# Kernel optimization log

Hardware: AMD Instinct MI355X
Metric: run time of the kernel (lower is better)

The kernel has to match this reference:

```python
import jax, jax.numpy as jnp
import numpy as np

L = 768          # temporal feature length
C_IN = 2048      # feature channels
NA = 10          # anchor scales per position
NC = 21          # num classes (20 + bg)
PRE_NMS = 1024   # pre-NMS top-k
POST_NMS = 128   # fixed proposal count after NMS
NMS_THR = 0.7
SCALE = 1.0      # cfg.Process.new_dilation*new_cluster/Frame
ANCHOR_SIZES = np.array([2., 4., 5., 6., 8., 9., 10., 12., 14., 16.], np.float32)


def _conv(x, w, b, pad=0):
    # x: [N,C,T], w: [O,I,K]
    y = jax.lax.conv_general_dilated(x, w, (1,), [(pad, pad)],
                                     dimension_numbers=('NCH', 'OIH', 'NCH'))
    return y + b[None, :, None]


def _lin(x, w, b):
    return x @ w.T + b


def _forward(feature, p):
    f = _conv(feature, p['w1f'], p['b1f'], 1)
    f = _conv(f, p['w2f'], p['b2f'], 1)
    x = _conv(f, p['wc1'], p['bc1'], 0)                      # [1,512,L]
    # SegmentProposal tower (relu only after conv4, as in source)
    h = _conv(x, p['sp1w'], p['sp1b'], 1)
    h = _conv(h, p['sp2w'], p['sp2b'], 1)
    h = _conv(h, p['sp3w'], p['sp3b'], 1)
    h = jax.nn.relu(_conv(h, p['sp4w'], p['sp4b'], 1))
    cls_score = _conv(h, p['spcw'], p['spcb'], 0)            # [1,2*NA,L]
    seg_pred = _conv(h, p['spsw'], p['spsb'], 0)             # [1,2*NA,L]

    def _resh(t):  # [1,2NA,L] -> [L*NA,2]  (transpose(2,1).view(B,L,C/2,2))
        return jnp.transpose(t, (0, 2, 1)).reshape(-1, 2)

    cls2 = _resh(cls_score)
    cls_prob = jax.nn.softmax(cls2, -1)
    off2 = _resh(seg_pred)

    # anchors: (center, half_len) per position per scale, position-major
    centers = (jnp.arange(L, dtype=jnp.float32) + 0.5) * SCALE
    halves = jnp.asarray(ANCHOR_SIZES) * 0.5
    a_c = jnp.repeat(centers, NA)
    a_h = jnp.tile(halves, L)
    im_info = L * SCALE

    # apply offsets: center shift + log-length scale, clip to video extent
    c = a_c + off2[:, 0] * (2.0 * a_h)
    hl = a_h * jnp.exp(off2[:, 1])
    s = jnp.clip(c - hl, 0.0, im_info)
    e = jnp.clip(c + hl, 0.0, im_info)
    scores = cls_prob[:, 1]

    top_sc, top_i = jax.lax.top_k(scores, PRE_NMS)
    ss, ee = s[top_i], e[top_i]

    def body(i, keep):
        inter = jnp.maximum(0., jnp.minimum(ee, ee[i]) - jnp.maximum(ss, ss[i]))
        union = (ee - ss) + (ee[i] - ss[i]) - inter
        iou = inter / jnp.maximum(union, 1e-8)
        sup = (iou > NMS_THR) & (jnp.arange(PRE_NMS) > i) & keep[i]
        return keep & ~sup

    keep = jax.lax.fori_loop(0, PRE_NMS, body, jnp.ones(PRE_NMS, bool))
    order = jnp.argsort((~keep).astype(jnp.int32), stable=True)  # kept first, score order
    sel = order[:POST_NMS]
    pidx = top_i[sel]
    ps, pe = s[pidx], e[pidx]
    pbbox = jnp.stack([(ps + pe) * 0.5, (pe - ps) * 0.5], -1)    # (center, half)

    # map proposals to feature index range (floor/ceil + clamp, as in source)
    st = jnp.clip(jnp.floor((pbbox[:, 0] - pbbox[:, 1]) / SCALE), 0, L - 1).astype(jnp.int32)
    en = jnp.clip(jnp.ceil((pbbox[:, 0] + pbbox[:, 1]) / SCALE), 0, L - 1).astype(jnp.int32)
    en = jnp.maximum(en, st)

    feat = f[0]                                              # [C_IN, L]
    tpos = jnp.arange(L)
    bins = jnp.arange(7)

    def roi_pool(se):  # AdaptiveMaxPool1d(7) over feat[:, s0:e0+1]
        s0, e0 = se
        ln = e0 - s0 + 1
        bs = s0 + (bins * ln) // 7
        be = s0 + ((bins + 1) * ln + 6) // 7 - 1
        m = (tpos[None, :] >= bs[:, None]) & (tpos[None, :] <= be[:, None])  # [7,L]
        v = jnp.where(m[None], feat[:, None, :], -jnp.inf)   # [C_IN,7,L]
        return v.max(-1)                                     # [C_IN,7]

    spp = jax.lax.map(roi_pool, (st, en))                    # [K,C_IN,7]

    y = _conv(spp, p['wc2'], p['bc2'], 0)
    y = _conv(y, p['w3'], p['b3'], 1)
    y = jax.nn.relu(_conv(y, p['w4'], p['b4'], 1))
    y = _conv(y, p['w5'], p['b5'], 1)
    y = jax.nn.relu(_conv(y, p['w6'], p['b6'], 1))
    y = y.reshape(y.shape[0], -1)                            # [K, 512*7]
    y = _lin(y, p['fc1w'], p['fc1b'])
    # Relation attention is computed but unused in the source forward -> omitted
    y = jax.nn.relu(y)
    y = _lin(y, p['fc2w'], p['fc2b'])
    y = _lin(y, p['fc3w'], p['fc3b'])
    obj_cls = _lin(y, p['clsw'], p['clsb'])                  # [K,NC]
    obj_off = _lin(y, p['boxw'], p['boxb']).reshape(-1, NC - 1, 2)
    cls_sel = cls2[pidx]                                     # [K,2]
    off_sel = off2[pidx]                                     # [K,2]
    return cls_sel, off_sel, obj_cls, obj_off


_PARAM_SHAPES = {
    'w1f': (2048, 2048, 3), 'b1f': (2048,),
    'w2f': (2048, 2048, 3), 'b2f': (2048,),
    'wc1': (512, 2048, 1), 'bc1': (512,),
    'sp1w': (512, 512, 3), 'sp1b': (512,),
    'sp2w': (512, 512, 3), 'sp2b': (512,),
    'sp3w': (512, 512, 3), 'sp3b': (512,),
    'sp4w': (512, 512, 3), 'sp4b': (512,),
    'spcw': (2 * NA, 512, 1), 'spcb': (2 * NA,),
    'spsw': (2 * NA, 512, 1), 'spsb': (2 * NA,),
    'wc2': (512, 2048, 1), 'bc2': (512,),
    'w3': (512, 512, 3), 'b3': (512,),
    'w4': (512, 512, 3), 'b4': (512,),
    'w5': (512, 512, 3), 'b5': (512,),
    'w6': (512, 512, 3), 'b6': (512,),
    'fc1w': (512, 512 * 7), 'fc1b': (512,),
    'fc2w': (256, 512), 'fc2b': (256,),
    'fc3w': (128, 256), 'fc3b': (128,),
    'clsw': (NC, 128), 'clsb': (NC,),
    'boxw': (2 * (NC - 1), 128), 'boxb': (2 * (NC - 1),),
}


def setup_inputs() -> dict:
    key = jax.random.key(0)
    inp = {'feature': jax.random.normal(jax.random.fold_in(key, 0), (1, C_IN, L), jnp.float32)}
    for i, (name, shp) in enumerate(sorted(_PARAM_SHAPES.items())):
        k = jax.random.fold_in(key, i + 1)
        inp[name] = jax.random.normal(k, shp, jnp.float32) * 0.02
    return inp


def reference(feature, b1f, b2f, b3, b4, b5, b6, bc1, bc2, boxb, boxw, clsb, clsw,
              fc1b, fc1w, fc2b, fc2w, fc3b, fc3w, sp1b, sp1w, sp2b, sp2w, sp3b, sp3w,
              sp4b, sp4w, spcb, spcw, spsb, spsw, w1f, w2f, w3, w4, w5, w6,
              wc1, wc2):
    p = dict(w1f=w1f, b1f=b1f, w2f=w2f, b2f=b2f, wc1=wc1, bc1=bc1,
             sp1w=sp1w, sp1b=sp1b, sp2w=sp2w, sp2b=sp2b, sp3w=sp3w, sp3b=sp3b,
             sp4w=sp4w, sp4b=sp4b, spcw=spcw, spcb=spcb, spsw=spsw, spsb=spsb,
             wc2=wc2, bc2=bc2, w3=w3, b3=b3, w4=w4, b4=b4, w5=w5, b5=b5,
             w6=w6, b6=b6, fc1w=fc1w, fc1b=fc1b, fc2w=fc2w, fc2b=fc2b,
             fc3w=fc3w, fc3b=fc3b, clsw=clsw, clsb=clsb, boxw=boxw, boxb=boxb)
    return _forward(feature, p)
```

## Files before the change

kernel.cpp:

```cpp
#include <hip/hip_runtime.h>

typedef __attribute__((ext_vector_type(8))) short short8;
typedef __attribute__((ext_vector_type(4))) float float4v;

__device__ __forceinline__ float bf(unsigned short u) {
    return __uint_as_float(((unsigned int)u) << 16);
}
__device__ __forceinline__ unsigned short f2b(float f) {
    unsigned int u = __float_as_uint(f);
    unsigned int r = (u + 0x7FFFu + ((u >> 16) & 1u)) >> 16;
    return (unsigned short)r;
}

__constant__ float c_anchors[10] = {2.f,4.f,5.f,6.f,8.f,9.f,10.f,12.f,14.f,16.f};

__global__ __launch_bounds__(256) void zeroXt_kernel(unsigned short* __restrict__ Xt, int CI) {
    int i = blockIdx.x * 256 + threadIdx.x;
    if (i < 2 * CI) {
        int row = (i >= CI) ? 769 : 0;
        int co = (i >= CI) ? (i - CI) : i;
        Xt[(size_t)row * CI + co] = 0;
        Xt[(size_t)770 * CI + (size_t)row * CI + co] = 0;
    }
}

__global__ __launch_bounds__(256) void decomp_kernel(const float* __restrict__ src,
                                                     unsigned short* __restrict__ Xt, int CI) {
    __shared__ float T[32][33];
    int l0 = blockIdx.x * 32, ci0 = blockIdx.y * 32;
    int tid = threadIdx.x;
#pragma unroll
    for (int i = 0; i < 4; i++) {
        int slot = tid + 256 * i;
        int r = slot >> 5, c = slot & 31;
        T[r][c] = src[(size_t)(ci0 + r) * 768 + l0 + c];
    }
    __syncthreads();
    unsigned short* Xh = Xt;
    unsigned short* Xl = Xt + (size_t)770 * CI;
#pragma unroll
    for (int i = 0; i < 4; i++) {
        int slot = tid + 256 * i;
        int li = slot >> 5, cc = slot & 31;
        float v = T[cc][li];
        unsigned short h = f2b(v);
        float lo = v - bf(h);
        size_t o = (size_t)(l0 + li + 1) * CI + ci0 + cc;
        Xh[o] = h;
        Xl[o] = f2b(lo);
    }
}

template <int TAPS, int SEGM>
__global__ __launch_bounds__(512, 6) void convmm_kernel(const float* __restrict__ W,
                                                        const unsigned short* __restrict__ Xt,
                                                        float* __restrict__ G,
                                                        int CO, int CI, int S, int NCOL, int planeElems) {
    constexpr int RS = TAPS * 32 + 8;
    constexpr int BROWS = SEGM ? 168 : 130;
    __shared__ unsigned short At[2][64 * RS];
    __shared__ unsigned short Bt[2][BROWS * 40];
    int tid = threadIdx.x;
    int lane = tid & 63, wid = tid >> 6;
    int q = lane >> 4, ln = lane & 15;
    int co0 = blockIdx.x * 64;
    int c0 = blockIdx.y * 128;
    int s = blockIdx.z;
    int kPer = CI / S, cis = s * kPer;
    const unsigned short* Xh = Xt;
    const unsigned short* Xl = Xt + planeElems;
    int row0 = SEGM ? ((c0 / 7) * 9 + c0 % 7) : c0;

    float4v zero4 = {0.f, 0.f, 0.f, 0.f};
    float4v acc[2][2];
    acc[0][0] = zero4; acc[0][1] = zero4; acc[1][0] = zero4; acc[1][1] = zero4;

    int wave_m = (wid >> 2) * 32;
    int wave_n = (wid & 3) * 32;

    int rowb[2];
#pragma unroll
    for (int nf = 0; nf < 2; nf++) {
        int col = c0 + wave_n + nf * 16 + ln;
        rowb[nf] = SEGM ? ((col / 7) * 9 + col % 7 - row0) : (wave_n + nf * 16 + ln);
    }

    for (int kb = 0; kb < kPer; kb += 32) {
        int cib = cis + kb;
        if (TAPS == 3) {
#pragma unroll
            for (int i = 0; i < 2; i++) {
                int slot = tid + 512 * i;
                int row = slot >> 4, cc0 = (slot & 15) * 2;
                const float* wp = W + ((size_t)(co0 + row) * CI + cib + cc0) * 3;
                float fa[6];
#pragma unroll
                for (int j = 0; j < 6; j++) fa[j] = wp[j];
#pragma unroll
                for (int t = 0; t < 3; t++) {
                    unsigned short h0 = f2b(fa[t]);
                    unsigned short h1 = f2b(fa[t + 3]);
                    unsigned short e0 = f2b(fa[t] - bf(h0));
                    unsigned short e1 = f2b(fa[t + 3] - bf(h1));
                    *(unsigned int*)&At[0][row * RS + t * 32 + cc0] =
                        (unsigned int)h0 | ((unsigned int)h1 << 16);
                    *(unsigned int*)&At[1][row * RS + t * 32 + cc0] =
                        (unsigned int)e0 | ((unsigned int)e1 << 16);
                }
            }
        } else {
            int row = tid >> 3, cc0 = (tid & 7) * 4;
            float4 wv = *(const float4*)(W + (size_t)(co0 + row) * CI + cib + cc0);
            float fa[4] = {wv.x, wv.y, wv.z, wv.w};
            unsigned short h[4], e[4];
#pragma unroll
            for (int j = 0; j < 4; j++) {
                h[j] = f2b(fa[j]);
                e[j] = f2b(fa[j] - bf(h[j]));
            }
            unsigned long long hp = (unsigned long long)h[0] | ((unsigned long long)h[1] << 16) |
                                    ((unsigned long long)h[2] << 32) | ((unsigned long long)h[3] << 48);
            unsigned long long ep = (unsigned long long)e[0] | ((unsigned long long)e[1] << 16) |
                                    ((unsigned long long)e[2] << 32) | ((unsigned long long)e[3] << 48);
            *(unsigned long long*)&At[0][row * RS + cc0] = hp;
            *(unsigned long long*)&At[1][row * RS + cc0] = ep;
        }
#pragma unroll
        for (int i = 0; i < 3; i++) {
            int slot = tid + 512 * i;
            if (slot < BROWS * 8) {
                int p = slot >= BROWS * 4 ? 1 : 0;
                int rem = slot - p * BROWS * 4;
                int r = rem >> 2, qq = rem & 3;
                const unsigned short* src = (p ? Xl : Xh) + (size_t)(row0 + r) * CI + cib + qq * 8;
                short8 v = *(const short8*)src;
                *(short8*)&Bt[p][r * 40 + qq * 8] = v;
            }
        }
        __syncthreads();
#pragma unroll
        for (int t = 0; t < TAPS; t++) {
            int shift = (TAPS == 1) ? 1 : t;
            short8 bh[2], bl[2];
#pragma unroll
            for (int nf = 0; nf < 2; nf++) {
                int rrow = rowb[nf] + shift;
                bh[nf] = *(const short8*)&Bt[0][rrow * 40 + q * 8];
                bl[nf] = *(const short8*)&Bt[1][rrow * 40 + q * 8];
            }
#pragma unroll
            for (int mf = 0; mf < 2; mf++) {
                int mrow = wave_m + mf * 16 + ln;
                short8 ah = *(const short8*)&At[0][mrow * RS + t * 32 + q * 8];
                short8 al = *(const short8*)&At[1][mrow * RS + t * 32 + q * 8];
#pragma unroll
                for (int nf = 0; nf < 2; nf++) {
                    acc[mf][nf] = __builtin_amdgcn_mfma_f32_16x16x32_bf16(ah, bh[nf], acc[mf][nf], 0, 0, 0);
                    acc[mf][nf] = __builtin_amdgcn_mfma_f32_16x16x32_bf16(ah, bl[nf], acc[mf][nf], 0, 0, 0);
                    acc[mf][nf] = __builtin_amdgcn_mfma_f32_16x16x32_bf16(al, bh[nf], acc[mf][nf], 0, 0, 0);
                }
            }
        }
        __syncthreads();
    }
    float* Gz = G + (size_t)s * CO * NCOL;
#pragma unroll
    for (int mf = 0; mf < 2; mf++)
#pragma unroll
        for (int nf = 0; nf < 2; nf++) {
            int col = c0 + wave_n + nf * 16 + ln;
            int rowb2 = co0 + wave_m + mf * 16 + q * 4;
#pragma unroll
            for (int r = 0; r < 4; r++)
                Gz[(size_t)(rowb2 + r) * NCOL + col] = acc[mf][nf][r];
        }
}

__global__ __launch_bounds__(256) void finsum_x_kernel(const float* __restrict__ G,
                                                       const float* __restrict__ bias,
                                                       unsigned short* __restrict__ Xt,
                                                       int CO, int P) {
    __shared__ float T[64][65];
    int co0 = blockIdx.x * 64, l0 = blockIdx.y * 64;
    int tid = threadIdx.x;
#pragma unroll 1
    for (int i = 0; i < 16; i++) {
        int slot = tid + 256 * i;
        int r = slot >> 6, c = slot & 63;
        float v = bias[co0 + r];
        for (int p = 0; p < P; p++) v += G[((size_t)p * CO + co0 + r) * 768 + l0 + c];
        T[r][c] = v;
    }
    __syncthreads();
    unsigned short* Xh = Xt;
    unsigned short* Xl = Xt + (size_t)770 * CO;
#pragma unroll 1
    for (int i = 0; i < 16; i++) {
        int slot = tid + 256 * i;
        int li = slot >> 6, ci = slot & 63;
        float v = T[ci][li];
        unsigned short h = f2b(v);
        float lo = v - bf(h);
        size_t o = (size_t)(l0 + li + 1) * CO + co0 + ci;
        Xh[o] = h;
        Xl[o] = f2b(lo);
    }
}

__global__ __launch_bounds__(256) void finsum_xf_kernel(const float* __restrict__ G,
                                                        const float* __restrict__ bias,
                                                        unsigned short* __restrict__ Xt,
                                                        float* __restrict__ outF,
                                                        int CO, int P) {
    __shared__ float T[64][65];
    int co0 = blockIdx.x * 64, l0 = blockIdx.y * 64;
    int tid = threadIdx.x;
#pragma unroll 1
    for (int i = 0; i < 16; i++) {
        int slot = tid + 256 * i;
        int r = slot >> 6, c = slot & 63;
        float v = bias[co0 + r];
        for (int p = 0; p < P; p++) v += G[((size_t)p * CO + co0 + r) * 768 + l0 + c];
        T[r][c] = v;
        outF[(size_t)(co0 + r) * 768 + l0 + c] = v;
    }
    __syncthreads();
    unsigned short* Xh = Xt;
    unsigned short* Xl = Xt + (size_t)770 * CO;
#pragma unroll 1
    for (int i = 0; i < 16; i++) {
        int slot = tid + 256 * i;
        int li = slot >> 6, ci = slot & 63;
        float v = T[ci][li];
        unsigned short h = f2b(v);
        float lo = v - bf(h);
        size_t o = (size_t)(l0 + li + 1) * CO + co0 + ci;
        Xh[o] = h;
        Xl[o] = f2b(lo);
    }
}

__global__ __launch_bounds__(256) void finsum_seg_kernel(const float* __restrict__ G,
                                                         const float* __restrict__ bias,
                                                         unsigned short* __restrict__ Xs,
                                                         int P, int relu) {
    __shared__ float T[64][65];
    int co0 = blockIdx.x * 64, c0 = blockIdx.y * 64;
    int tid = threadIdx.x;
#pragma unroll 1
    for (int i = 0; i < 16; i++) {
        int slot = tid + 256 * i;
        int r = slot >> 6, c = slot & 63;
        float v = bias[co0 + r];
        for (int p = 0; p < P; p++) v += G[((size_t)p * 512 + co0 + r) * 896 + c0 + c];
        if (relu) v = fmaxf(v, 0.f);
        T[r][c] = v;
    }
    __syncthreads();
    unsigned short* Xh = Xs;
    unsigned short* Xl = Xs + (size_t)1160 * 512;
#pragma unroll 1
    for (int i = 0; i < 16; i++) {
        int slot = tid + 256 * i;
        int li = slot >> 6, ci = slot & 63;
        float v = T[ci][li];
        int c = c0 + li;
        int row = (c / 7) * 9 + c % 7 + 1;
        unsigned short h = f2b(v);
        float lo = v - bf(h);
        size_t o = (size_t)row * 512 + co0 + ci;
        Xh[o] = h;
        Xl[o] = f2b(lo);
    }
}

__global__ __launch_bounds__(256) void finsum_f_kernel(const float* __restrict__ G,
                                                       const float* __restrict__ bias,
                                                       float* __restrict__ out,
                                                       int CO, int P, int ncol, int relu) {
    int i = blockIdx.x * 256 + threadIdx.x;
    if (i >= CO * ncol) return;
    int r = i / ncol, c = i - r * ncol;
    float v = bias[r];
    for (int p = 0; p < P; p++) v += G[((size_t)p * CO + r) * ncol + c];
    if (relu) v = fmaxf(v, 0.f);
    out[i] = v;
}

__global__ __launch_bounds__(256) void finalize_kernel(const float* __restrict__ part,
                                                       float* __restrict__ out,
                                                       const float* __restrict__ bias,
                                                       int RPAD, int R, int NCOLS, int S, int relu) {
    int i = blockIdx.x * 256 + threadIdx.x;
    int total = R * NCOLS;
    if (i >= total) return;
    int r = i / NCOLS;
    int c = i - r * NCOLS;
    float v = 0.f;
    for (int s = 0; s < S; s++) v += part[((size_t)s * RPAD + r) * NCOLS + c];
    v += bias[r];
    if (relu) v = fmaxf(v, 0.f);
    out[i] = v;
}

template <int MODE, int EPI>
__global__ __launch_bounds__(256) void gemm_kernel(const float* __restrict__ W,
                                                   const float* __restrict__ B,
                                                   const float* __restrict__ bias,
                                                   float* __restrict__ outF,
                                                   int R, int K, int NCOLS, int LDB, int S, int relu) {
    __shared__ __align__(16) float Bt[16][68];
    __shared__ __align__(16) float Wt[16][68];
    int tid = threadIdx.x;
    int tx = tid & 15, ty = tid >> 4;
    int r0 = blockIdx.x * 64, c0 = blockIdx.y * 64, s = blockIdx.z;
    int kPer = K / S;
    int k0s = s * kPer;
    float acc[4][4] = {};
    for (int kb = 0; kb < kPer; kb += 16) {
        int k0 = k0s + kb;
        {
            int rr = r0 + (tid >> 2);
            int q = tid & 3;
            float4 wv4 = {0.f, 0.f, 0.f, 0.f};
            if (rr < R) wv4 = *(const float4*)(W + (size_t)rr * K + k0 + q * 4);
            Wt[q * 4 + 0][tid >> 2] = wv4.x;
            Wt[q * 4 + 1][tid >> 2] = wv4.y;
            Wt[q * 4 + 2][tid >> 2] = wv4.z;
            Wt[q * 4 + 3][tid >> 2] = wv4.w;
        }
#pragma unroll
        for (int p = 0; p < 4; p++) {
            int kk = p * 4 + (tid >> 6);
            int c = tid & 63;
            int k = k0 + kk;
            int col = c0 + c;
            float v;
            if (MODE == 0) {
                v = B[(size_t)k * LDB + col];
            } else {
                int co = k / 7;
                int b7 = k - co * 7;
                v = B[(size_t)co * 896 + col * 7 + b7];
            }
            Bt[kk][c] = v;
        }
        __syncthreads();
#pragma unroll
        for (int kk = 0; kk < 16; kk++) {
            float4 bv = *(const float4*)&Bt[kk][tx * 4];
            float4 wv = *(const float4*)&Wt[kk][ty * 4];
            float bb[4] = {bv.x, bv.y, bv.z, bv.w};
            float ww[4] = {wv.x, wv.y, wv.z, wv.w};
#pragma unroll
            for (int i = 0; i < 4; i++)
#pragma unroll
                for (int j = 0; j < 4; j++)
                    acc[i][j] = fmaf(ww[i], bb[j], acc[i][j]);
        }
        __syncthreads();
    }
    if (EPI == 0) {
        if (S > 1) {
#pragma unroll
            for (int i = 0; i < 4; i++) {
                int r = r0 + ty * 4 + i;
                float4 o = {acc[i][0], acc[i][1], acc[i][2], acc[i][3]};
                *(float4*)&outF[((size_t)s * R + r) * NCOLS + c0 + tx * 4] = o;
            }
        } else {
#pragma unroll
            for (int i = 0; i < 4; i++) {
                int r = r0 + ty * 4 + i;
                if (r < R) {
                    float bv = bias[r];
#pragma unroll
                    for (int j = 0; j < 4; j++) {
                        float v = acc[i][j] + bv;
                        if (relu) v = fmaxf(v, 0.f);
                        outF[(size_t)r * NCOLS + c0 + tx * 4 + j] = v;
                    }
                }
            }
        }
    } else {
#pragma unroll
        for (int i = 0; i < 4; i++) {
            int r = r0 + ty * 4 + i;
            if (r < R) {
                float bv = bias[r];
#pragma unroll
                for (int j = 0; j < 4; j++) {
                    int col = c0 + tx * 4 + j;
                    float v = acc[i][j] + bv;
                    if (EPI == 1) outF[512 + col * 21 + r] = v;
                    else outF[3200 + col * 40 + r] = v;
                }
            }
        }
    }
}

__global__ __launch_bounds__(256) void proposal_kernel(const float* __restrict__ clsS,
                                                       const float* __restrict__ segS,
                                                       float* __restrict__ cls2, float* __restrict__ off2,
                                                       float* __restrict__ scores,
                                                       float* __restrict__ sArr, float* __restrict__ eArr) {
    int i = blockIdx.x * 256 + threadIdx.x;
    if (i >= 7680) return;
    int l = i / 10;
    int a = i - l * 10;
    float c0 = clsS[(a * 2 + 0) * 768 + l];
    float c1 = clsS[(a * 2 + 1) * 768 + l];
    cls2[i * 2] = c0;
    cls2[i * 2 + 1] = c1;
    float m = fmaxf(c0, c1);
    float e0 = expf(c0 - m), e1 = expf(c1 - m);
    scores[i] = e1 / (e0 + e1);
    float o0 = segS[(a * 2 + 0) * 768 + l];
    float o1 = segS[(a * 2 + 1) * 768 + l];
    off2[i * 2] = o0;
    off2[i * 2 + 1] = o1;
    float ah = c_anchors[a] * 0.5f;
    float ac = (float)l + 0.5f;
    float c = ac + o0 * (2.f * ah);
    float hl = ah * expf(o1);
    sArr[i] = fminf(fmaxf(c - hl, 0.f), 768.f);
    eArr[i] = fminf(fmaxf(c + hl, 0.f), 768.f);
}

__global__ __launch_bounds__(1024) void sortA_kernel(const float* __restrict__ scores,
                                                     unsigned long long* __restrict__ runs) {
    __shared__ unsigned long long kk[1024];
    int tid = threadIdx.x;
    int gbase = blockIdx.x * 1024;
    int gi = gbase + tid;
    unsigned long long key = 0ull;
    if (gi < 7680) {
        unsigned int sb = __float_as_uint(scores[gi]);
        key = ((unsigned long long)sb << 32) | (unsigned long long)(0xFFFFFFFFu - (unsigned)gi);
    }
    kk[tid] = key;
    __syncthreads();
    for (int k = 2; k <= 1024; k <<= 1) {
        for (int j = k >> 1; j > 0; j >>= 1) {
            int ixj = tid ^ j;
            if (ixj > tid) {
                unsigned long long a = kk[tid], b = kk[ixj];
                bool descend = ((tid & k) == 0);
                if (descend ? (a < b) : (a > b)) { kk[tid] = b; kk[ixj] = a; }
            }
            __syncthreads();
        }
    }
    runs[gbase + tid] = kk[tid];
}

__global__ __launch_bounds__(1024) void sortB_kernel(const unsigned long long* __restrict__ runs,
                                                     const float* __restrict__ sArr, const float* __restrict__ eArr,
                                                     int* __restrict__ topI,
                                                     float* __restrict__ ss, float* __restrict__ ee) {
    __shared__ unsigned long long S[8192];
    int tid = threadIdx.x;
#pragma unroll
    for (int m = 0; m < 8; m++) S[m * 1024 + tid] = runs[m * 1024 + tid];
    __syncthreads();
#pragma unroll 1
    for (int level = 0; level < 3; level++) {
        int span = 1024 << level;
        int nm = 4 >> level;
        for (int m = 0; m < nm; m++) {
            int baseA = m * (span * 2);
            int baseB = baseA + span;
            unsigned long long a = S[baseA + tid], b = S[baseB + 1023 - tid];
            S[baseA + tid] = (a > b) ? a : b;
        }
        __syncthreads();
        for (int j = 512; j > 0; j >>= 1) {
            for (int m = 0; m < nm; m++) {
                int baseA = m * (span * 2);
                int ixj = tid ^ j;
                if (ixj > tid) {
                    unsigned long long a = S[baseA + tid], b = S[baseA + ixj];
                    if (a < b) { S[baseA + tid] = b; S[baseA + ixj] = a; }
                }
            }
            __syncthreads();
        }
    }
    int idx = (int)(0xFFFFFFFFu - (unsigned int)(S[tid] & 0xFFFFFFFFull));
    topI[tid] = idx;
    ss[tid] = sArr[idx];
    ee[tid] = eArr[idx];
}

__global__ __launch_bounds__(256) void nms_mask_kernel(const float* __restrict__ ss, const float* __restrict__ ee,
                                                       unsigned long long* __restrict__ mask) {
    int g = blockIdx.x * 256 + threadIdx.x;
    int i = g >> 4, w = g & 15;
    float si = ss[i], ei = ee[i];
    unsigned long long bits = 0ull;
#pragma unroll 1
    for (int jj = 0; jj < 64; jj++) {
        int j = w * 64 + jj;
        if (j > i) {
            float sj = ss[j], ej = ee[j];
            float inter = fmaxf(0.f, fminf(ei, ej) - fmaxf(si, sj));
            float uni = (ej - sj) + (ei - si) - inter;
            float iou = inter / fmaxf(uni, 1e-8f);
            if (iou > 0.7f) bits |= (1ull << jj);
        }
    }
    mask[(size_t)i * 16 + w] = bits;
}

__device__ __forceinline__ unsigned long long readlane64(unsigned long long v, int i) {
    unsigned int lo = (unsigned int)__builtin_amdgcn_readlane((int)(unsigned int)(v & 0xFFFFFFFFull), i);
    unsigned int hi = (unsigned int)__builtin_amdgcn_readlane((int)(unsigned int)(v >> 32), i);
    return ((unsigned long long)hi << 32) | (unsigned long long)lo;
}

__global__ __launch_bounds__(64) void nms_select_kernel(const unsigned long long* __restrict__ mask,
                                                        const int* __restrict__ topI,
                                                        const float* __restrict__ ss, const float* __restrict__ ee,
                                                        const float* __restrict__ cls2, const float* __restrict__ off2,
                                                        int* __restrict__ stA, int* __restrict__ enA,
                                                        float* __restrict__ out) {
    int lane = threadIdx.x;
    unsigned long long keepW[16];
#pragma unroll 1
    for (int b = 0; b < 16; b++) {
        unsigned long long accv = 0ull;
#pragma unroll 1
        for (int a = 0; a < b; a++) {
            unsigned long long m = mask[(size_t)(a * 64 + lane) * 16 + b];
            unsigned long long kb = (keepW[a] >> lane) & 1ull;
            accv |= m & (0ull - kb);
        }
#pragma unroll
        for (int sft = 1; sft < 64; sft <<= 1) accv |= __shfl_xor(accv, sft);
        unsigned long long diag = mask[(size_t)(b * 64 + lane) * 16 + b];
        unsigned long long rem = accv;
#pragma unroll
        for (int i = 0; i < 64; i++) {
            unsigned long long di = readlane64(diag, i);
            if (!((rem >> i) & 1ull)) rem |= di;
        }
        keepW[b] = ~rem;
    }
    int total = 0;
    int prefix[16];
#pragma unroll
    for (int b = 0; b < 16; b++) { prefix[b] = total; total += __popcll(keepW[b]); }
#pragma unroll 1
    for (int b = 0; b < 16; b++) {
        int tid = b * 64 + lane;
        unsigned long long keep64 = keepW[b];
        unsigned long long below = (lane == 0) ? 0ull : (keep64 << (64 - lane));
        int keptBefore = prefix[b] + __popcll(below);
        int kp = (int)((keep64 >> lane) & 1ull);
        int pos = kp ? keptBefore : (total + tid - keptBefore);
        if (pos < 128) {
            int orig = topI[tid];
            float ps = ss[tid], pe = ee[tid];
            out[pos * 2 + 0] = cls2[orig * 2 + 0];
            out[pos * 2 + 1] = cls2[orig * 2 + 1];
            out[256 + pos * 2 + 0] = off2[orig * 2 + 0];
            out[256 + pos * 2 + 1] = off2[orig * 2 + 1];
            float bc = (ps + pe) * 0.5f, bh = (pe - ps) * 0.5f;
            int st = (int)fminf(fmaxf(floorf(bc - bh), 0.f), 767.f);
            int en = (int)fminf(fmaxf(ceilf(bc + bh), 0.f), 767.f);
            if (en < st) en = st;
            stA[pos] = st;
            enA[pos] = en;
        }
    }
}

__global__ __launch_bounds__(256) void roi_slab_kernel(const float* __restrict__ f,
                                                       const int* __restrict__ stA, const int* __restrict__ enA,
                                                       unsigned short* __restrict__ Xs) {
    int col = blockIdx.x;
    int n = col / 7, b = col - n * 7;
    int st = stA[n], en = enA[n];
    int ln = en - st + 1;
    int bs = st + (b * ln) / 7;
    int be = st + ((b + 1) * ln + 6) / 7 - 1;
    unsigned short* Xh = Xs;
    unsigned short* Xl = Xs + (size_t)898 * 2048;
    int tid = threadIdx.x;
#pragma unroll 1
    for (int j = 0; j < 8; j++) {
        int ci = tid + 256 * j;
        const float* row = f + (size_t)ci * 768;
        float m = row[bs];
        for (int t = bs + 1; t <= be; t++) m = fmaxf(m, row[t]);
        unsigned short h = f2b(m);
        float lo = m - bf(h);
        size_t o = (size_t)(col + 1) * 2048 + ci;
        Xh[o] = h;
        Xl[o] = f2b(lo);
    }
}

__global__ __launch_bounds__(256) void zrow_wc2_kernel(unsigned short* __restrict__ Xs) {
    int i = blockIdx.x * 256 + threadIdx.x;
    if (i < 2048) {
        Xs[i] = 0;
        Xs[(size_t)897 * 2048 + i] = 0;
        Xs[(size_t)898 * 2048 + i] = 0;
        Xs[(size_t)898 * 2048 + (size_t)897 * 2048 + i] = 0;
    }
}

__global__ __launch_bounds__(256) void zseg_kernel(uint4* __restrict__ p, int n16) {
    int i = blockIdx.x * 256 + threadIdx.x;
    uint4 z = {0, 0, 0, 0};
    if (i < n16) p[i] = z;
}

extern "C" void kernel_launch(void* const* d_in, const int* in_sizes, int n_in,
                              void* d_out, int out_size, void* d_ws, size_t ws_size,
                              hipStream_t stream) {
    const float* IN[39];
    for (int i = 0; i < 39; i++) IN[i] = (const float*)d_in[i];
    const float* feature = IN[0];
    const float *b1f = IN[1], *b2f = IN[2], *b3 = IN[3], *b4 = IN[4], *b5 = IN[5], *b6 = IN[6];
    const float *bc1 = IN[7], *bc2 = IN[8], *boxb = IN[9], *boxw = IN[10];
    const float *clsb = IN[11], *clsw = IN[12];
    const float *fc1b = IN[13], *fc1w = IN[14], *fc2b = IN[15], *fc2w = IN[16];
    const float *fc3b = IN[17], *fc3w = IN[18];
    const float *sp1b = IN[19], *sp1w = IN[20], *sp2b = IN[21], *sp2w = IN[22];
    const float *sp3b = IN[23], *sp3w = IN[24], *sp4b = IN[25], *sp4w = IN[26];
    const float *spcb = IN[27], *spcw = IN[28], *spsb = IN[29], *spsw = IN[30];
    const float *w1f = IN[31], *w2f = IN[32], *w3w = IN[33], *w4w = IN[34];
    const float *w5w = IN[35], *w6w = IN[36], *wc1 = IN[37], *wc2 = IN[38];
    float* out = (float*)d_out;

    char* base = (char*)d_ws;
    float* G    = (float*)base;
    float* part = (float*)base;
    unsigned short* segSA = (unsigned short*)(base + 14680064);
    unsigned short* segSB = (unsigned short*)(base + 17055744);
    float* yA   = (float*)(base + 22020096);
    float* g1   = (float*)(base + 25690112);
    float* g2   = (float*)(base + 25952256);
    float* g3   = (float*)(base + 26083328);
    size_t off = 26148864;
    auto alloc = [&](size_t bytes) { void* p = base + off; off += (bytes + 15) & ~((size_t)15); return p; };
    unsigned short* Xt = (unsigned short*)alloc((size_t)770 * 2048 * 2 * 2);
    float* fbuf = (float*)alloc((size_t)2048 * 768 * 4);
    float* hB   = (float*)alloc((size_t)512 * 768 * 4);
    float* clsS = (float*)alloc((size_t)20 * 768 * 4);
    float* segS = (float*)alloc((size_t)20 * 768 * 4);
    float* cls2 = (float*)alloc(7680 * 2 * 4);
    float* off2 = (float*)alloc(7680 * 2 * 4);
    float* scores = (float*)alloc(7680 * 4);
    float* sArr = (float*)alloc(7680 * 4);
    float* eArr = (float*)alloc(7680 * 4);
    float* ssS  = (float*)alloc(1024 * 4);
    float* eeS  = (float*)alloc(1024 * 4);
    unsigned long long* runs = (unsigned long long*)alloc((size_t)8192 * 8);
    unsigned long long* mask = (unsigned long long*)alloc((size_t)16384 * 8);
    int* topI = (int*)alloc(1024 * 4);
    int* stA = (int*)alloc(128 * 4);
    int* enA = (int*)alloc(128 * 4);

    dim3 blk(256);
    dim3 blk512(512);

    zeroXt_kernel<<<16, blk, 0, stream>>>(Xt, 2048);
    decomp_kernel<<<dim3(24, 64), blk, 0, stream>>>(feature, Xt, 2048);
    convmm_kernel<3, 0><<<dim3(32, 6, 4), blk512, 0, stream>>>(w1f, Xt, G, 2048, 2048, 4, 768, 770 * 2048);
    finsum_x_kernel<<<dim3(32, 12), blk, 0, stream>>>(G, b1f, Xt, 2048, 4);
    convmm_kernel<3, 0><<<dim3(32, 6, 4), blk512, 0, stream>>>(w2f, Xt, G, 2048, 2048, 4, 768, 770 * 2048);
    finsum_xf_kernel<<<dim3(32, 12), blk, 0, stream>>>(G, b2f, Xt, fbuf, 2048, 4);

    convmm_kernel<1, 0><<<dim3(8, 6, 8), blk512, 0, stream>>>(wc1, Xt, G, 512, 2048, 8, 768, 770 * 2048);
    zeroXt_kernel<<<4, blk, 0, stream>>>(Xt, 512);
    finsum_x_kernel<<<dim3(8, 12), blk, 0, stream>>>(G, bc1, Xt, 512, 8);

    convmm_kernel<3, 0><<<dim3(8, 6, 8), blk512, 0, stream>>>(sp1w, Xt, G, 512, 512, 8, 768, 770 * 512);
    finsum_x_kernel<<<dim3(8, 12), blk, 0, stream>>>(G, sp1b, Xt, 512, 8);
    convmm_kernel<3, 0><<<dim3(8, 6, 8), blk512, 0, stream>>>(sp2w, Xt, G, 512, 512, 8, 768, 770 * 512);
    finsum_x_kernel<<<dim3(8, 12), blk, 0, stream>>>(G, sp2b, Xt, 512, 8);
    convmm_kernel<3, 0><<<dim3(8, 6, 8), blk512, 0, stream>>>(sp3w, Xt, G, 512, 512, 8, 768, 770 * 512);
    finsum_x_kernel<<<dim3(8, 12), blk, 0, stream>>>(G, sp3b, Xt, 512, 8);
    convmm_kernel<3, 0><<<dim3(8, 6, 8), blk512, 0, stream>>>(sp4w, Xt, G, 512, 512, 8, 768, 770 * 512);
    finsum_f_kernel<<<1536, blk, 0, stream>>>(G, sp4b, hB, 512, 8, 768, 1);

    gemm_kernel<0, 0><<<dim3(1, 12, 1), blk, 0, stream>>>(spcw, hB, spcb, clsS, 20, 512, 768, 768, 1, 0);
    gemm_kernel<0, 0><<<dim3(1, 12, 1), blk, 0, stream>>>(spsw, hB, spsb, segS, 20, 512, 768, 768, 1, 0);

    proposal_kernel<<<30, blk, 0, stream>>>(clsS, segS, cls2, off2, scores, sArr, eArr);
    sortA_kernel<<<8, 1024, 0, stream>>>(scores, runs);
    sortB_kernel<<<1, 1024, 0, stream>>>(runs, sArr, eArr, topI, ssS, eeS);
    nms_mask_kernel<<<64, blk, 0, stream>>>(ssS, eeS, mask);
    nms_select_kernel<<<1, 64, 0, stream>>>(mask, topI, ssS, eeS, cls2, off2, stA, enA, out);

    zrow_wc2_kernel<<<8, blk, 0, stream>>>(Xt);
    roi_slab_kernel<<<896, blk, 0, stream>>>(fbuf, stA, enA, Xt);
    zseg_kernel<<<1160, blk, 0, stream>>>((uint4*)segSA, 296960);

    convmm_kernel<1, 0><<<dim3(8, 7, 8), blk512, 0, stream>>>(wc2, Xt, G, 512, 2048, 8, 896, 898 * 2048);
    finsum_seg_kernel<<<dim3(8, 14), blk, 0, stream>>>(G, bc2, segSA, 8, 0);
    convmm_kernel<3, 1><<<dim3(8, 7, 8), blk512, 0, stream>>>(w3w, segSA, G, 512, 512, 8, 896, 1160 * 512);
    finsum_seg_kernel<<<dim3(8, 14), blk, 0, stream>>>(G, b3, segSB, 8, 0);
    convmm_kernel<3, 1><<<dim3(8, 7, 8), blk512, 0, stream>>>(w4w, segSB, G, 512, 512, 8, 896, 1160 * 512);
    finsum_seg_kernel<<<dim3(8, 14), blk, 0, stream>>>(G, b4, segSA, 8, 1);
    convmm_kernel<3, 1><<<dim3(8, 7, 8), blk512, 0, stream>>>(w5w, segSA, G, 512, 512, 8, 896, 1160 * 512);
    finsum_seg_kernel<<<dim3(8, 14), blk, 0, stream>>>(G, b5, segSB, 8, 0);
    convmm_kernel<3, 1><<<dim3(8, 7, 8), blk512, 0, stream>>>(w6w, segSB, G, 512, 512, 8, 896, 1160 * 512);
    finsum_f_kernel<<<1792, blk, 0, stream>>>(G, b6, yA, 512, 8, 896, 1);

    gemm_kernel<1, 0><<<dim3(8, 2, 28), blk, 0, stream>>>(fc1w, yA, fc1b, part, 512, 3584, 128, 128, 28, 0);
    finalize_kernel<<<256, blk, 0, stream>>>(part, g1, fc1b, 512, 512, 128, 28, 1);

    gemm_kernel<0, 0><<<dim3(4, 2, 4), blk, 0, stream>>>(fc2w, g1, fc2b, part, 256, 512, 128, 128, 4, 0);
    finalize_kernel<<<128, blk, 0, stream>>>(part, g2, fc2b, 256, 256, 128, 4, 0);
    gemm_kernel<0, 0><<<dim3(2, 2, 2), blk, 0, stream>>>(fc3w, g2, fc3b, part, 128, 256, 128, 128, 2, 0);
    finalize_kernel<<<64, blk, 0, stream>>>(part, g3, fc3b, 128, 128, 128, 2, 0);

    gemm_kernel<0, 1><<<dim3(1, 2, 1), blk, 0, stream>>>(clsw, g3, clsb, out, 21, 128, 128, 128, 1, 0);
    gemm_kernel<0, 2><<<dim3(1, 2, 1), blk, 0, stream>>>(boxw, g3, boxb, out, 40, 128, 128, 128, 1, 0);
}
```

Before: 1.029 ms.

## Pre-split conv weights into bf16 hi/lo planes and load MFMA operands directly

Adds a repack kernel that splits each fp32 conv weight into bf16 high and low residual planes laid out tap-major per output channel. The convolution kernel then reads A fragments straight from global memory into registers, so it no longer converts weights or stages them through LDS on every k-step. This removes per-block redundant conversion and LDS traffic, but adds a full weight pass per layer and uncoalesced-ish per-lane global loads. It also splits the small classifier GEMMs over K with a finalize pass and enlarges workspace allocations, with a fallback when the big buffer does not fit.

```diff
diff --git a/kernel.cpp b/kernel.cpp
--- a/kernel.cpp
+++ b/kernel.cpp
@@ -13,6 +13,25 @@
 }
 
 __constant__ float c_anchors[10] = {2.f,4.f,5.f,6.f,8.f,9.f,10.f,12.f,14.f,16.f};
+
+__global__ __launch_bounds__(256) void repackW_kernel(const float* __restrict__ W,
+                                                      unsigned short* __restrict__ Wr,
+                                                      int CO, int CI, int TAPS) {
+    int i = blockIdx.x * 256 + threadIdx.x;
+    int n = CO * CI * TAPS;
+    if (i >= n) return;
+    int cit = CI * TAPS;
+    int co = i / cit;
+    int rem = i - co * cit;
+    int ci = rem / TAPS;
+    int t = rem - ci * TAPS;
+    float v = W[i];
+    unsigned short h = f2b(v);
+    unsigned short l = f2b(v - bf(h));
+    size_t o = ((size_t)(co * TAPS + t) * 2) * CI + ci;
+    Wr[o] = h;
+    Wr[o + CI] = l;
+}
 
 __global__ __launch_bounds__(256) void zeroXt_kernel(unsigned short* __restrict__ Xt, int CI) {
     int i = blockIdx.x * 256 + threadIdx.x;
@@ -52,13 +71,11 @@
 }
 
 template <int TAPS, int SEGM>
-__global__ __launch_bounds__(512, 6) void convmm_kernel(const float* __restrict__ W,
-                                                        const unsigned short* __restrict__ Xt,
-                                                        float* __restrict__ G,
-                                                        int CO, int CI, int S, int NCOL, int planeElems) {
-    constexpr int RS = TAPS * 32 + 8;
+__global__ __launch_bounds__(512, 6) void convmmW_kernel(const unsigned short* __restrict__ Wr,
+                                                         const unsigned short* __restrict__ Xt,
+                                                         float* __restrict__ G,
+                                                         int CO, int CI, int S, int NCOL, int planeElems) {
     constexpr int BROWS = SEGM ? 168 : 130;
-    __shared__ unsigned short At[2][64 * RS];
     __shared__ unsigned short Bt[2][BROWS * 40];
     int tid = threadIdx.x;
     int lane = tid & 63, wid = tid >> 6;
@@ -78,6 +95,12 @@
     int wave_m = (wid >> 2) * 32;
     int wave_n = (wid & 3) * 32;
 
+    size_t wbase[2];
+#pragma unroll
+    for (int mf = 0; mf < 2; mf++) {
+        int row = co0 + wave_m + mf * 16 + ln;
+        wbase[mf] = ((size_t)row * TAPS) * 2 * CI + q * 8;
+    }
     int rowb[2];
 #pragma unroll
     for (int nf = 0; nf < 2; nf++) {
@@ -87,44 +110,6 @@
 
     for (int kb = 0; kb < kPer; kb += 32) {
         int cib = cis + kb;
-        if (TAPS == 3) {
-#pragma unroll
-            for (int i = 0; i < 2; i++) {
-                int slot = tid + 512 * i;
-                int row = slot >> 4, cc0 = (slot & 15) * 2;
-                const float* wp = W + ((size_t)(co0 + row) * CI + cib + cc0) * 3;
-                float fa[6];
-#pragma unroll
-                for (int j = 0; j < 6; j++) fa[j] = wp[j];
-#pragma unroll
-                for (int t = 0; t < 3; t++) {
-                    unsigned short h0 = f2b(fa[t]);
-                    unsigned short h1 = f2b(fa[t + 3]);
-                    unsigned short e0 = f2b(fa[t] - bf(h0));
-                    unsigned short e1 = f2b(fa[t + 3] - bf(h1));
-                    *(unsigned int*)&At[0][row * RS + t * 32 + cc0] =
-                        (unsigned int)h0 | ((unsigned int)h1 << 16);
-                    *(unsigned int*)&At[1][row * RS + t * 32 + cc0] =
-                        (unsigned int)e0 | ((unsigned int)e1 << 16);
-                }
-            }
-        } else {
-            int row = tid >> 3, cc0 = (tid & 7) * 4;
-            float4 wv = *(const float4*)(W + (size_t)(co0 + row) * CI + cib + cc0);
-            float fa[4] = {wv.x, wv.y, wv.z, wv.w};
-            unsigned short h[4], e[4];
-#pragma unroll
-            for (int j = 0; j < 4; j++) {
-                h[j] = f2b(fa[j]);
-                e[j] = f2b(fa[j] - bf(h[j]));
-            }
-            unsigned long long hp = (unsigned long long)h[0] | ((unsigned long long)h[1] << 16) |
-                                    ((unsigned long long)h[2] << 32) | ((unsigned long long)h[3] << 48);
-            unsigned long long ep = (unsigned long long)e[0] | ((unsigned long long)e[1] << 16) |
-                                    ((unsigned long long)e[2] << 32) | ((unsigned long long)e[3] << 48);
-            *(unsigned long long*)&At[0][row * RS + cc0] = hp;
-            *(unsigned long long*)&At[1][row * RS + cc0] = ep;
-        }
 #pragma unroll
         for (int i = 0; i < 3; i++) {
             int slot = tid + 512 * i;
@@ -141,10 +126,109 @@
 #pragma unroll
         for (int t = 0; t < TAPS; t++) {
             int shift = (TAPS == 1) ? 1 : t;
+            short8 ah[2], al[2];
+#pragma unroll
+            for (int mf = 0; mf < 2; mf++) {
+                const unsigned short* pa = Wr + wbase[mf] + (size_t)(t * 2) * CI + cib;
+                ah[mf] = *(const short8*)pa;
+                al[mf] = *(const short8*)(pa + CI);
+            }
             short8 bh[2], bl[2];
 #pragma unroll
             for (int nf = 0; nf < 2; nf++) {
                 int rrow = rowb[nf] + shift;
+                bh[nf] = *(const short8*)&Bt[0][rrow * 40 + q * 8];
+                bl[nf] = *(const short8*)&Bt[1][rrow * 40 + q * 8];
+            }
+#pragma unroll
+            for (int mf = 0; mf < 2; mf++)
+#pragma unroll
+                for (int nf = 0; nf < 2; nf++) {
+                    acc[mf][nf] = __builtin_amdgcn_mfma_f32_16x16x32_bf16(ah[mf], bh[nf], acc[mf][nf], 0, 0, 0);
+                    acc[mf][nf] = __builtin_amdgcn_mfma_f32_16x16x32_bf16(ah[mf], bl[nf], acc[mf][nf], 0, 0, 0);
+                    acc[mf][nf] = __builtin_amdgcn_mfma_f32_16x16x32_bf16(al[mf], bh[nf], acc[mf][nf], 0, 0, 0);
+                }
+        }
+        __syncthreads();
+    }
+    float* Gz = G + (size_t)s * CO * NCOL;
+#pragma unroll
+    for (int mf = 0; mf < 2; mf++)
+#pragma unroll
+        for (int nf = 0; nf < 2; nf++) {
+            int col = c0 + wave_n + nf * 16 + ln;
+            int rowb2 = co0 + wave_m + mf * 16 + q * 4;
+#pragma unroll
+            for (int r = 0; r < 4; r++)
+                Gz[(size_t)(rowb2 + r) * NCOL + col] = acc[mf][nf][r];
+        }
+}
+
+__global__ __launch_bounds__(512, 6) void convmm_kernel(const float* __restrict__ W,
+                                                        const unsigned short* __restrict__ Xt,
+                                                        float* __restrict__ G,
+                                                        int CO, int CI, int S, int NCOL, int planeElems) {
+    constexpr int RS = 3 * 32 + 8;
+    __shared__ unsigned short At[2][64 * RS];
+    __shared__ unsigned short Bt[2][130 * 40];
+    int tid = threadIdx.x;
+    int lane = tid & 63, wid = tid >> 6;
+    int q = lane >> 4, ln = lane & 15;
+    int co0 = blockIdx.x * 64;
+    int c0 = blockIdx.y * 128;
+    int s = blockIdx.z;
+    int kPer = CI / S, cis = s * kPer;
+    const unsigned short* Xh = Xt;
+    const unsigned short* Xl = Xt + planeElems;
+
+    float4v zero4 = {0.f, 0.f, 0.f, 0.f};
+    float4v acc[2][2];
+    acc[0][0] = zero4; acc[0][1] = zero4; acc[1][0] = zero4; acc[1][1] = zero4;
+
+    int wave_m = (wid >> 2) * 32;
+    int wave_n = (wid & 3) * 32;
+
+    for (int kb = 0; kb < kPer; kb += 32) {
+        int cib = cis + kb;
+#pragma unroll
+        for (int i = 0; i < 2; i++) {
+            int slot = tid + 512 * i;
+            int row = slot >> 4, cc0 = (slot & 15) * 2;
+            const float* wp = W + ((size_t)(co0 + row) * CI + cib + cc0) * 3;
+            float fa[6];
+#pragma unroll
+            for (int j = 0; j < 6; j++) fa[j] = wp[j];
+#pragma unroll
+            for (int t = 0; t < 3; t++) {
+                unsigned short h0 = f2b(fa[t]);
+                unsigned short h1 = f2b(fa[t + 3]);
+                unsigned short e0 = f2b(fa[t] - bf(h0));
+                unsigned short e1 = f2b(fa[t + 3] - bf(h1));
+                *(unsigned int*)&At[0][row * RS + t * 32 + cc0] =
+                    (unsigned int)h0 | ((unsigned int)h1 << 16);
+                *(unsigned int*)&At[1][row * RS + t * 32 + cc0] =
+                    (unsigned int)e0 | ((unsigned int)e1 << 16);
+            }
+        }
+#pragma unroll
+        for (int i = 0; i < 3; i++) {
+            int slot = tid + 512 * i;
+            if (slot < 1040) {
+                int p = slot >= 520 ? 1 : 0;
+                int rem = slot - p * 520;
+                int r = rem >> 2, qq = rem & 3;
+                const unsigned short* src = (p ? Xl : Xh) + (size_t)(c0 + r) * CI + cib + qq * 8;
+                short8 v = *(const short8*)src;
+                *(short8*)&Bt[p][r * 40 + qq * 8] = v;
+            }
+        }
+        __syncthreads();
+#pragma unroll
+        for (int t = 0; t < 3; t++) {
+            short8 bh[2], bl[2];
+#pragma unroll
+            for (int nf = 0; nf < 2; nf++) {
+                int rrow = wave_n + nf * 16 + ln + t;
                 bh[nf] = *(const short8*)&Bt[0][rrow * 40 + q * 8];
                 bl[nf] = *(const short8*)&Bt[1][rrow * 40 + q * 8];
             }
@@ -365,8 +449,10 @@
 #pragma unroll
             for (int i = 0; i < 4; i++) {
                 int r = r0 + ty * 4 + i;
-                float4 o = {acc[i][0], acc[i][1], acc[i][2], acc[i][3]};
-                *(float4*)&outF[((size_t)s * R + r) * NCOLS + c0 + tx * 4] = o;
+                if (r < R) {
+                    float4 o = {acc[i][0], acc[i][1], acc[i][2], acc[i][3]};
+                    *(float4*)&outF[((size_t)s * R + r) * NCOLS + c0 + tx * 4] = o;
+                }
             }
         } else {
 #pragma unroll
@@ -640,6 +726,7 @@
     char* base = (char*)d_ws;
     float* G    = (float*)base;
     float* part = (float*)base;
+    unsigned short* WrSmall = (unsigned short*)(base + 14680064);
     unsigned short* segSA = (unsigned short*)(base + 14680064);
     unsigned short* segSB = (unsigned short*)(base + 17055744);
     float* yA   = (float*)(base + 22020096);
@@ -647,9 +734,11 @@
     float* g2   = (float*)(base + 25952256);
     float* g3   = (float*)(base + 26083328);
     size_t off = 26148864;
-    auto alloc = [&](size_t bytes) { void* p = base + off; off += (bytes + 15) & ~((size_t)15); return p; };
-    unsigned short* Xt = (unsigned short*)alloc((size_t)770 * 2048 * 2 * 2);
+    auto alloc = [&](size_t bytes) { void* p = base + off; off += (bytes + 63) & ~((size_t)63); return p; };
+    unsigned short* Xt = (unsigned short*)alloc((size_t)898 * 2048 * 2 * 2);
     float* fbuf = (float*)alloc((size_t)2048 * 768 * 4);
+    unsigned short* WrWc2 = (unsigned short*)fbuf;
+    unsigned short* WrTower = (unsigned short*)Xt;
     float* hB   = (float*)alloc((size_t)512 * 768 * 4);
     float* clsS = (float*)alloc((size_t)20 * 768 * 4);
     float* segS = (float*)alloc((size_t)20 * 768 * 4);
@@ -666,31 +755,52 @@
     int* stA = (int*)alloc(128 * 4);
     int* enA = (int*)alloc(128 * 4);
 
+    size_t bigWrBytes = (size_t)2048 * 3 * 2 * 2048 * 2;
+    unsigned short* WrBig = (unsigned short*)alloc(bigWrBytes);
+    bool useBigWr = (off <= ws_size);
+
     dim3 blk(256);
     dim3 blk512(512);
 
     zeroXt_kernel<<<16, blk, 0, stream>>>(Xt, 2048);
     decomp_kernel<<<dim3(24, 64), blk, 0, stream>>>(feature, Xt, 2048);
-    convmm_kernel<3, 0><<<dim3(32, 6, 4), blk512, 0, stream>>>(w1f, Xt, G, 2048, 2048, 4, 768, 770 * 2048);
+    if (useBigWr) {
+        repackW_kernel<<<49152, blk, 0, stream>>>(w1f, WrBig, 2048, 2048, 3);
+        convmmW_kernel<3, 0><<<dim3(32, 6, 4), blk512, 0, stream>>>(WrBig, Xt, G, 2048, 2048, 4, 768, 770 * 2048);
+    } else {
+        convmm_kernel<<<dim3(32, 6, 4), blk512, 0, stream>>>(w1f, Xt, G, 2048, 2048, 4, 768, 770 * 2048);
+    }
     finsum_x_kernel<<<dim3(32, 12), blk, 0, stream>>>(G, b1f, Xt, 2048, 4);
-    convmm_kernel<3, 0><<<dim3(32, 6, 4), blk512, 0, stream>>>(w2f, Xt, G, 2048, 2048, 4, 768, 770 * 2048);
+    if (useBigWr) {
+        repackW_kernel<<<49152, blk, 0, stream>>>(w2f, WrBig, 2048, 2048, 3);
+        convmmW_kernel<3, 0><<<dim3(32, 6, 4), blk512, 0, stream>>>(WrBig, Xt, G, 2048, 2048, 4, 768, 770 * 2048);
+    } else {
+        convmm_kernel<<<dim3(32, 6, 4), blk512, 0, stream>>>(w2f, Xt, G, 2048, 2048, 4, 768, 770 * 2048);
+    }
     finsum_xf_kernel<<<dim3(32, 12), blk, 0, stream>>>(G, b2f, Xt, fbuf, 2048, 4);
 
-    convmm_kernel<1, 0><<<dim3(8, 6, 8), blk512, 0, stream>>>(wc1, Xt, G, 512, 2048, 8, 768, 770 * 2048);
+    repackW_kernel<<<4096, blk, 0, stream>>>(wc1, WrSmall, 512, 2048, 1);
+    convmmW_kernel<1, 0><<<dim3(8, 6, 8), blk512, 0, stream>>>(WrSmall, Xt, G, 512, 2048, 8, 768, 770 * 2048);
     zeroXt_kernel<<<4, blk, 0, stream>>>(Xt, 512);
     finsum_x_kernel<<<dim3(8, 12), blk, 0, stream>>>(G, bc1, Xt, 512, 8);
 
-    convmm_kernel<3, 0><<<dim3(8, 6, 8), blk512, 0, stream>>>(sp1w, Xt, G, 512, 512, 8, 768, 770 * 512);
+    repackW_kernel<<<3072, blk, 0, stream>>>(sp1w, WrSmall, 512, 512, 3);
+    convmmW_kernel<3, 0><<<dim3(8, 6, 8), blk512, 0, stream>>>(WrSmall, Xt, G, 512, 512, 8, 768, 770 * 512);
     finsum_x_kernel<<<dim3(8, 12), blk, 0, stream>>>(G, sp1b, Xt, 512, 8);
-    convmm_kernel<3, 0><<<dim3(8, 6, 8), blk512, 0, stream>>>(sp2w, Xt, G, 512, 512, 8, 768, 770 * 512);
+    repackW_kernel<<<3072, blk, 0, stream>>>(sp2w, WrSmall, 512, 512, 3);
+    convmmW_kernel<3, 0><<<dim3(8, 6, 8), blk512, 0, stream>>>(WrSmall, Xt, G, 512, 512, 8, 768, 770 * 512);
     finsum_x_kernel<<<dim3(8, 12), blk, 0, stream>>>(G, sp2b, Xt, 512, 8);
-    convmm_kernel<3, 0><<<dim3(8, 6, 8), blk512, 0, stream>>>(sp3w, Xt, G, 512, 512, 8, 768, 770 * 512);
+    repackW_kernel<<<3072, blk, 0, stream>>>(sp3w, WrSmall, 512, 512, 3);
+    convmmW_kernel<3, 0><<<dim3(8, 6, 8), blk512, 0, stream>>>(WrSmall, Xt, G, 512, 512, 8, 768, 770 * 512);
     finsum_x_kernel<<<dim3(8, 12), blk, 0, stream>>>(G, sp3b, Xt, 512, 8);
-    convmm_kernel<3, 0><<<dim3(8, 6, 8), blk512, 0, stream>>>(sp4w, Xt, G, 512, 512, 8, 768, 770 * 512);
+    repackW_kernel<<<3072, blk, 0, stream>>>(sp4w, WrSmall, 512, 512, 3);
+    convmmW_kernel<3, 0><<<dim3(8, 6, 8), blk512, 0, stream>>>(WrSmall, Xt, G, 512, 512, 8, 768, 770 * 512);
     finsum_f_kernel<<<1536, blk, 0, stream>>>(G, sp4b, hB, 512, 8, 768, 1);
 
-    gemm_kernel<0, 0><<<dim3(1, 12, 1), blk, 0, stream>>>(spcw, hB, spcb, clsS, 20, 512, 768, 768, 1, 0);
-    gemm_kernel<0, 0><<<dim3(1, 12, 1), blk, 0, stream>>>(spsw, hB, spsb, segS, 20, 512, 768, 768, 1, 0);
+    gemm_kernel<0, 0><<<dim3(1, 12, 8), blk, 0, stream>>>(spcw, hB, spcb, part, 20, 512, 768, 768, 8, 0);
+    finalize_kernel<<<60, blk, 0, stream>>>(part, clsS, spcb, 20, 20, 768, 8, 0);
+    gemm_kernel<0, 0><<<dim3(1, 12, 8), blk, 0, stream>>>(spsw, hB, spsb, part, 20, 512, 768, 768, 8, 0);
+    finalize_kernel<<<60, blk, 0, stream>>>(part, segS, spsb, 20, 20, 768, 8, 0);
 
     proposal_kernel<<<30, blk, 0, stream>>>(clsS, segS, cls2, off2, scores, sArr, eArr);
     sortA_kernel<<<8, 1024, 0, stream>>>(scores, runs);
@@ -702,15 +812,20 @@
     roi_slab_kernel<<<896, blk, 0, stream>>>(fbuf, stA, enA, Xt);
     zseg_kernel<<<1160, blk, 0, stream>>>((uint4*)segSA, 296960);
 
-    convmm_kernel<1, 0><<<dim3(8, 7, 8), blk512, 0, stream>>>(wc2, Xt, G, 512, 2048, 8, 896, 898 * 2048);
+    repackW_kernel<<<4096, blk, 0, stream>>>(wc2, WrWc2, 512, 2048, 1);
+    convmmW_kernel<1, 0><<<dim3(8, 7, 8), blk512, 0, stream>>>(WrWc2, Xt, G, 512, 2048, 8, 896, 898 * 2048);
     finsum_seg_kernel<<<dim3(8, 14), blk, 0, stream>>>(G, bc2, segSA, 8, 0);
-    convmm_kernel<3, 1><<<dim3(8, 7, 8), blk512, 0, stream>>>(w3w, segSA, G, 512, 512, 8, 896, 1160 * 512);
+    repackW_kernel<<<3072, blk, 0, stream>>>(w3w, WrTower, 512, 512, 3);
+    convmmW_kernel<3, 1><<<dim3(8, 7, 8), blk512, 0, stream>>>(WrTower, segSA, G, 512, 512, 8, 896, 1160 * 512);
     finsum_seg_kernel<<<dim3(8, 14), blk, 0, stream>>>(G, b3, segSB, 8, 0);
-    convmm_kernel<3, 1><<<dim3(8, 7, 8), blk512, 0, stream>>>(w4w, segSB, G, 512, 512, 8, 896, 1160 * 512);
+    repackW_kernel<<<3072, blk, 0, stream>>>(w4w, WrTower, 512, 512, 3);
+    convmmW_kernel<3, 1><<<dim3(8, 7, 8), blk512, 0, stream>>>(WrTower, segSB, G, 512, 512, 8, 896, 1160 * 512);
     finsum_seg_kernel<<<dim3(8, 14), blk, 0, stream>>>(G, b4, segSA, 8, 1);
-    convmm_kernel<3, 1><<<dim3(8, 7, 8), blk512, 0, stream>>>(w5w, segSA, G, 512, 512, 8, 896, 1160 * 512);
+    repackW_kernel<<<3072, blk, 0, stream>>>(w5w, WrTower, 512, 512, 3);
+    convmmW_kernel<3, 1><<<dim3(8, 7, 8), blk512, 0, stream>>>(WrTower, segSA, G, 512, 512, 8, 896, 1160 * 512);
     finsum_seg_kernel<<<dim3(8, 14), blk, 0, stream>>>(G, b5, segSB, 8, 0);
-    convmm_kernel<3, 1><<<dim3(8, 7, 8), blk512, 0, stream>>>(w6w, segSB, G, 512, 512, 8, 896, 1160 * 512);
+    repackW_kernel<<<3072, blk, 0, stream>>>(w6w, WrTower, 512, 512, 3);
+    convmmW_kernel<3, 1><<<dim3(8, 7, 8), blk512, 0, stream>>>(WrTower, segSB, G, 512, 512, 8, 896, 1160 * 512);
     finsum_f_kernel<<<1792, blk, 0, stream>>>(G, b6, yA, 512, 8, 896, 1);
 
     gemm_kernel<1, 0><<<dim3(8, 2, 28), blk, 0, stream>>>(fc1w, yA, fc1b, part, 512, 3584, 128, 128, 28, 0);
```

Result: slower. 1.341 ms (+30.2%).
